# Kernel optimization log

Measured on AMD Instinct MI355X. Metric: run time of the kernel, lower is better.

Reference implementation:

```python
import jax, jax.numpy as jnp
import numpy as np
from jax import lax

STRIDES = (8, 8, 16, 32, 32)
GRIDS = (40, 36, 24, 16, 12)
MIN_SCORE = 0.1
KEEP_SCORE = 0.1
MASK_THR = 0.5
UPDATE_THR = 0.05
SIGMA = 2.0
TOPN = 500
MAX_MASKS = 100
UP = 4


def points_nms(h):
    # max_pool2d(k=2, s=1, p=1) then crop last row/col == pad (1,0) window 2
    m = lax.reduce_window(h, -jnp.inf, lax.max, (1, 1, 2, 2), (1, 1, 1, 1),
                          ((0, 0), (0, 0), (1, 0), (1, 0)))
    return h * (m == h).astype(h.dtype)


def resize_mat(insz, outsz):
    # bilinear align_corners=True interpolation matrix [outsz, insz]
    if outsz > 1:
        src = jnp.arange(outsz, dtype=jnp.float32) * ((insz - 1) / (outsz - 1))
    else:
        src = jnp.zeros((outsz,), jnp.float32)
    lo = jnp.clip(jnp.floor(src).astype(jnp.int32), 0, insz - 1)
    hi = jnp.minimum(lo + 1, insz - 1)
    w = src - lo.astype(jnp.float32)
    r = jnp.arange(outsz)
    M = jnp.zeros((outsz, insz), jnp.float32)
    return M.at[r, lo].add(1.0 - w).at[r, hi].add(w)


def bilinear(x, oh, ow):  # x: [k,h,w]
    Mh = resize_mat(x.shape[1], oh)
    Mw = resize_mat(x.shape[2], ow)
    return jnp.einsum('Ww,kHw->kHW', Mw, jnp.einsum('Hh,khw->kHw', Mh, x))


def prep(cate_preds, kernel_preds):
    B = cate_preds[0].shape[0]
    cate = [points_nms(jax.nn.sigmoid(c)) for c in cate_preds]
    cate_flat = jnp.concatenate(
        [jnp.transpose(c, (0, 2, 3, 1)).reshape(B, -1, c.shape[1]) for c in cate], axis=1)
    kern_flat = jnp.concatenate(
        [jnp.transpose(k, (0, 2, 3, 1)).reshape(B, -1, k.shape[1]) for k in kernel_preds], axis=1)
    strides_vec = jnp.concatenate(
        [jnp.full((g * g,), float(s), jnp.float32) for g, s in zip(GRIDS, STRIDES)])
    return cate_flat, kern_flat, strides_vec


def decode_soft(mask_feat, cate_flat, kern_flat, strides_vec):
    # fixed-shape (padded) version of the per-image decode; invalid slots carry score 0
    nc = cate_flat.shape[-1]
    flat = cate_flat.reshape(-1)
    vals, idx = lax.top_k(jnp.where(flat > MIN_SCORE, flat, -1.0), TOPN)
    validk = vals > MIN_SCORE
    cell = idx // nc
    label = idx % nc
    # dynamic 1x1 conv == einsum with gathered kernels
    sig = jax.nn.sigmoid(jnp.einsum('kc,chw->khw', kern_flat[cell], mask_feat))
    binm = (sig > MASK_THR).astype(sig.dtype)
    summ = binm.sum((1, 2))
    keep = validk & (summ > strides_vec[cell])
    seg = (sig * binm).sum((1, 2)) / jnp.maximum(summ, 1e-6)
    scores = jnp.where(keep, vals * seg, 0.0)
    order = jnp.argsort(-scores)
    scores = scores[order]
    sig = sig[order]
    label = label[order]
    keep_o = keep[order]
    summ = jnp.where(keep, summ, 0.0)[order]
    binm = binm[order] * keep_o[:, None, None].astype(binm.dtype)
    # matrix NMS (gaussian)
    flatm = binm.reshape(TOPN, -1)
    inter = flatm @ flatm.T
    iou = inter / jnp.maximum(summ[:, None] + summ[None, :] - inter, 1e-6)
    triu = jnp.triu(jnp.ones((TOPN, TOPN), bool), 1)
    dmat = jnp.where(triu & (label[:, None] == label[None, :]), iou, 0.0)
    comp = dmat.max(0)  # max suppression each item received
    coef = (jnp.exp(-SIGMA * dmat**2) / jnp.exp(-SIGMA * comp[:, None]**2)).min(0)
    s2 = scores * coef
    s2 = jnp.where((s2 >= UPDATE_THR) & (s2 >= KEEP_SCORE) & keep_o, s2, 0.0)
    fv, fi = lax.top_k(s2, MAX_MASKS)
    return fv, jnp.where(fv > 0, label[fi], -1), sig[fi]


def reference(mask_feat_pred, cate_pred_0, cate_pred_1, cate_pred_2, cate_pred_3,
              cate_pred_4, kernel_pred_0, kernel_pred_1, kernel_pred_2, kernel_pred_3,
              kernel_pred_4, scaled_sizes, origin_sizes):
    cate_preds = [cate_pred_0, cate_pred_1, cate_pred_2, cate_pred_3, cate_pred_4]
    kernel_preds = [kernel_pred_0, kernel_pred_1, kernel_pred_2, kernel_pred_3, kernel_pred_4]
    cate_flat, kern_flat, sv = prep(cate_preds, kernel_preds)
    fv, lab, sig = jax.vmap(lambda mf, cf, kf: decode_soft(mf, cf, kf, sv))(
        mask_feat_pred, cate_flat, kern_flat)
    H = mask_feat_pred.shape[2] * UP
    W = mask_feat_pred.shape[3] * UP
    up = jax.vmap(lambda s: bilinear(s, H, W))(sig)  # [B,M,H,W]
    sh, sw = int(scaled_sizes[0, 0]), int(scaled_sizes[0, 1])
    oh, ow = int(origin_sizes[0, 0]), int(origin_sizes[0, 1])
    up = up[:, :, :sh, :sw]
    up = jax.vmap(lambda s: bilinear(s, oh, ow))(up)
    masks = ((up > MASK_THR) & (fv > 0)[:, :, None, None]).astype(jnp.uint8)
    return masks, lab, fv


def setup_inputs() -> dict:
    key = jax.random.key(0)
    ks = jax.random.split(key, 11)
    B, C, NC, HM = 2, 256, 80, 128
    inp = {'mask_feat_pred': jax.random.normal(ks[0], (B, C, HM, HM), jnp.float32)}
    for i, g in enumerate(GRIDS):
        inp[f'cate_pred_{i}'] = jax.random.normal(ks[1 + i], (B, NC, g, g), jnp.float32)
        inp[f'kernel_pred_{i}'] = jax.random.normal(ks[6 + i], (B, C, g, g), jnp.float32) * 0.05
    inp['scaled_sizes'] = jnp.full((B, 2), HM * UP, jnp.int32)
    inp['origin_sizes'] = jnp.full((B, 2), HM * UP, jnp.int32)
    return inp
```

## Files before the change

kernel.cpp:

```cpp
#include <hip/hip_runtime.h>
#include <math.h>
#include <stdint.h>

#define NBATCH 2
#define NC 80
#define CHN 256
#define HMM 128
#define HWN (HMM*HMM)
#define NCELL 3872
#define FLATN (NCELL*NC)
#define TOPN 500
#define SROWS 512
#define MAXM 100
#define OUTH 512
#define OUTW 512
#define NBINS 1024
#define CANDCAP 2048
#define BM 128
#define BN2 256
#define BK 32
#define GNB (HWN/BN2)

__device__ __forceinline__ float sigmoidf_(float x){ return 1.0f/(1.0f+expf(-x)); }

__device__ __forceinline__ void cell_decode(int cell, int& lvl, int& g, int& y, int& x){
  int off;
  if (cell < 1600)      { lvl=0; g=40; off=0; }
  else if (cell < 2896) { lvl=1; g=36; off=1600; }
  else if (cell < 3472) { lvl=2; g=24; off=2896; }
  else if (cell < 3728) { lvl=3; g=16; off=3472; }
  else                  { lvl=4; g=12; off=3728; }
  int r = cell - off; y = r / g; x = r - y*g;
}

template<int N, int NT>
__device__ __forceinline__ void bitonic_desc(uint64_t* key){
  int tid = threadIdx.x;
  for (int k = 2; k <= N; k <<= 1)
    for (int j = k >> 1; j > 0; j >>= 1) {
      __syncthreads();
      for (int e = tid; e < N; e += NT) {
        int l = e ^ j;
        if (l > e) {
          uint64_t a = key[e], c = key[l];
          bool up = ((e & k) == 0);
          if (up ? (a < c) : (a > c)) { key[e] = c; key[l] = a; }
        }
      }
    }
  __syncthreads();
}

__global__ void k0_init(uint32_t* hist, uint32_t* cnt){
  int t = blockIdx.x*blockDim.x + threadIdx.x;
  if (t < NBATCH*NBINS) hist[t] = 0;
  if (t < NBATCH) cnt[t] = 0;
}

__global__ void k1_scores(const float* __restrict__ c0, const float* __restrict__ c1,
                          const float* __restrict__ c2, const float* __restrict__ c3,
                          const float* __restrict__ c4,
                          float* __restrict__ scores, uint32_t* __restrict__ hist){
  int t = blockIdx.x*blockDim.x + threadIdx.x;
  if (t >= NBATCH*FLATN) return;
  int b = t / FLATN;
  int rem = t - b*FLATN;
  int cell = rem / NC;
  int c = rem - cell*NC;
  int lvl,g,y,x; cell_decode(cell,lvl,g,y,x);
  const float* cp = lvl==0?c0:lvl==1?c1:lvl==2?c2:lvl==3?c3:c4;
  const float* base = cp + (size_t)(b*NC + c)*g*g;
  float raw = base[y*g + x];
  float m = raw;
  if (y > 0)          m = fmaxf(m, base[(y-1)*g + x]);
  if (x > 0)          m = fmaxf(m, base[y*g + x-1]);
  if (y > 0 && x > 0) m = fmaxf(m, base[(y-1)*g + x-1]);
  float s = (raw == m) ? sigmoidf_(raw) : 0.0f;
  scores[t] = s;
  if (s > 0.1f) {
    int bin = (int)(s * 1024.0f); if (bin > NBINS-1) bin = NBINS-1;
    atomicAdd(&hist[b*NBINS + bin], 1u);
  }
}

__global__ __launch_bounds__(1024) void k2_cutoff(const uint32_t* __restrict__ hist, int* __restrict__ cutoff){
  __shared__ uint32_t h[NBINS];
  int b = blockIdx.x;
  h[threadIdx.x] = hist[b*NBINS + threadIdx.x];
  __syncthreads();
  if (threadIdx.x == 0) {
    int acc = 0; int cut = 0;
    for (int d = NBINS-1; d >= 0; --d) {
      acc += (int)h[d];
      if (acc >= TOPN) { cut = d; break; }
    }
    cutoff[b] = cut;
  }
}

__global__ void k3_gather(const float* __restrict__ scores, const int* __restrict__ cutoff,
                          uint32_t* __restrict__ cnt, float* __restrict__ cval, uint32_t* __restrict__ cidx){
  int t = blockIdx.x*blockDim.x + threadIdx.x;
  if (t >= NBATCH*FLATN) return;
  int b = t / FLATN; int idx = t - b*FLATN;
  float v = scores[t];
  if (v > 0.1f) {
    int bin = (int)(v * 1024.0f); if (bin > NBINS-1) bin = NBINS-1;
    if (bin >= cutoff[b]) {
      uint32_t p = atomicAdd(&cnt[b], 1u);
      if (p < CANDCAP) { cval[b*CANDCAP+p] = v; cidx[b*CANDCAP+p] = (uint32_t)idx; }
    }
  }
}

__global__ __launch_bounds__(1024) void k4_sort(const uint32_t* __restrict__ cnt,
        const float* __restrict__ cval, const uint32_t* __restrict__ cidx,
        float* __restrict__ vals, int* __restrict__ cellA, int* __restrict__ labelA){
  __shared__ uint64_t key[CANDCAP];
  int b = blockIdx.x; int tid = threadIdx.x;
  int n = (int)cnt[b]; if (n > CANDCAP) n = CANDCAP;
  for (int e = tid; e < CANDCAP; e += 1024) {
    uint64_t k = 0;
    if (e < n)
      k = ((uint64_t)__float_as_uint(cval[b*CANDCAP+e]) << 32) |
          (uint64_t)(0xFFFFFFFFu - cidx[b*CANDCAP+e]);
    key[e] = k;
  }
  bitonic_desc<CANDCAP,1024>(key);
  for (int r = tid; r < TOPN; r += 1024) {
    uint64_t k = key[r];
    if ((k >> 32) == 0) { vals[b*TOPN+r] = -1.0f; cellA[b*TOPN+r] = 0; labelA[b*TOPN+r] = 0; }
    else {
      uint32_t idx = 0xFFFFFFFFu - (uint32_t)(k & 0xFFFFFFFFu);
      vals[b*TOPN+r]   = __uint_as_float((uint32_t)(k >> 32));
      cellA[b*TOPN+r]  = (int)(idx / NC);
      labelA[b*TOPN+r] = (int)(idx % NC);
    }
  }
}

__global__ void k5_kmat(const float* __restrict__ k0p, const float* __restrict__ k1p,
                        const float* __restrict__ k2p, const float* __restrict__ k3p,
                        const float* __restrict__ k4p,
                        const int* __restrict__ cellA, float* __restrict__ Kmat){
  int t = blockIdx.x*blockDim.x + threadIdx.x;
  if (t >= NBATCH*TOPN*CHN) return;
  int b = t / (TOPN*CHN); int rem = t - b*(TOPN*CHN);
  int k = rem / CHN; int c = rem - k*CHN;
  int cell = cellA[b*TOPN + k];
  int lvl,g,y,x; cell_decode(cell,lvl,g,y,x);
  const float* kp = lvl==0?k0p:lvl==1?k1p:lvl==2?k2p:lvl==3?k3p:k4p;
  Kmat[t] = kp[((size_t)(b*CHN + c)*g + y)*g + x];
}

__global__ __launch_bounds__(256, 2) void k6_gemm1(const float* __restrict__ Kmat, const float* __restrict__ mf,
        float* __restrict__ sigfull, uint32_t* __restrict__ bits,
        float* __restrict__ psum, float* __restrict__ pseg){
  __shared__ alignas(16) float As[BK][BM+4];
  __shared__ alignas(16) float Bs[BK][BN2];
  __shared__ uint32_t bitsL[BM][8];
  int tid = threadIdx.x;
  int nb = blockIdx.x, mb = blockIdx.y, b = blockIdx.z;
  int row0 = mb*BM, col0 = nb*BN2;
  int tx = tid & 15, ty = tid >> 4;
  for (int i = tid; i < BM*8; i += 256) ((uint32_t*)bitsL)[i] = 0;

  int ar[4], aq[4], bkk[8], bcc[8];
  #pragma unroll
  for (int i = 0; i < 4; ++i) { int e = i*256 + tid; ar[i] = e >> 3; aq[i] = e & 7; }
  #pragma unroll
  for (int i = 0; i < 8; ++i) { int e = i*256 + tid; bkk[i] = e >> 6; bcc[i] = e & 63; }

  float4 pa[4], pb[8];
  const float4 z4 = make_float4(0.f,0.f,0.f,0.f);
  #pragma unroll
  for (int i = 0; i < 4; ++i) {
    int rr = row0 + ar[i];
    pa[i] = (rr < TOPN) ? *(const float4*)&Kmat[((size_t)b*TOPN + rr)*CHN + aq[i]*4] : z4;
  }
  #pragma unroll
  for (int i = 0; i < 8; ++i)
    pb[i] = *(const float4*)&mf[((size_t)b*CHN + bkk[i])*HWN + col0 + bcc[i]*4];

  float acc[8][16];
  #pragma unroll
  for (int i=0;i<8;i++)
    #pragma unroll
    for(int j=0;j<16;j++) acc[i][j]=0.f;

  for (int k0 = 0; k0 < CHN; k0 += BK) {
    __syncthreads();
    #pragma unroll
    for (int i = 0; i < 4; ++i) {
      int colA = ar[i] ^ (aq[i] << 2);
      As[aq[i]*4+0][colA] = pa[i].x;
      As[aq[i]*4+1][colA] = pa[i].y;
      As[aq[i]*4+2][colA] = pa[i].z;
      As[aq[i]*4+3][colA] = pa[i].w;
    }
    #pragma unroll
    for (int i = 0; i < 8; ++i)
      *(float4*)&Bs[bkk[i]][bcc[i]*4] = pb[i];
    __syncthreads();
    if (k0 + BK < CHN) {
      int k0n = k0 + BK;
      #pragma unroll
      for (int i = 0; i < 4; ++i) {
        int rr = row0 + ar[i];
        pa[i] = (rr < TOPN) ? *(const float4*)&Kmat[((size_t)b*TOPN + rr)*CHN + k0n + aq[i]*4] : z4;
      }
      #pragma unroll
      for (int i = 0; i < 8; ++i)
        pb[i] = *(const float4*)&mf[((size_t)b*CHN + k0n + bkk[i])*HWN + col0 + bcc[i]*4];
    }
    #pragma unroll 2
    for (int kk = 0; kk < BK; ++kk) {
      int s = (kk >> 2) << 2;
      float4 a0 = *(float4*)&As[kk][(ty*8) ^ s];
      float4 a1 = *(float4*)&As[kk][(ty*8+4) ^ s];
      float av[8] = {a0.x,a0.y,a0.z,a0.w,a1.x,a1.y,a1.z,a1.w};
      #pragma unroll
      for (int q = 0; q < 4; ++q) {
        float4 bv = *(float4*)&Bs[kk][q*64 + tx*4];
        #pragma unroll
        for (int i = 0; i < 8; ++i) {
          acc[i][q*4+0] += av[i]*bv.x;
          acc[i][q*4+1] += av[i]*bv.y;
          acc[i][q*4+2] += av[i]*bv.z;
          acc[i][q*4+3] += av[i]*bv.w;
        }
      }
    }
  }
  #pragma unroll
  for (int i = 0; i < 8; ++i) {
    int r = row0 + ty*8 + i;
    float se = 0.f; int cc = 0;
    #pragma unroll
    for (int q = 0; q < 4; ++q) {
      float4 sv;
      sv.x = sigmoidf_(acc[i][q*4+0]);
      sv.y = sigmoidf_(acc[i][q*4+1]);
      sv.z = sigmoidf_(acc[i][q*4+2]);
      sv.w = sigmoidf_(acc[i][q*4+3]);
      uint32_t m = 0;
      if (sv.x > 0.5f) { m |= 1u; se += sv.x; cc++; }
      if (sv.y > 0.5f) { m |= 2u; se += sv.y; cc++; }
      if (sv.z > 0.5f) { m |= 4u; se += sv.z; cc++; }
      if (sv.w > 0.5f) { m |= 8u; se += sv.w; cc++; }
      atomicOr(&bitsL[ty*8+i][2*q + (tx>>3)], m << ((tx&7)*4));
      *(float4*)&sigfull[((size_t)b*SROWS + r)*HWN + col0 + q*64 + tx*4] = sv;
    }
    #pragma unroll
    for (int d = 1; d < 16; d <<= 1) {
      se += __shfl_xor(se, d);
      cc += __shfl_xor(cc, d);
    }
    if (tx == 0 && r < TOPN) {
      psum[((size_t)b*TOPN + r)*GNB + nb] = (float)cc;
      pseg[((size_t)b*TOPN + r)*GNB + nb] = se;
    }
  }
  __syncthreads();
  for (int e = tid; e < BM*8; e += 256) {
    int rr = e >> 3, w = e & 7;
    if (row0 + rr < TOPN)
      bits[((size_t)b*TOPN + row0 + rr)*512 + nb*8 + w] = bitsL[rr][w];
  }
}

__global__ void k7_rowstats(const float* __restrict__ psum, const float* __restrict__ pseg,
                            const float* __restrict__ vals, const int* __restrict__ cellA,
                            float* __restrict__ summ, float* __restrict__ scores, int* __restrict__ keepA){
  int t = blockIdx.x*blockDim.x + threadIdx.x;
  if (t >= NBATCH*TOPN) return;
  float sc = 0.f, sg = 0.f;
  for (int i = 0; i < GNB; i += 4) {
    float4 a = *(const float4*)&psum[(size_t)t*GNB+i];
    float4 c = *(const float4*)&pseg[(size_t)t*GNB+i];
    sc += a.x+a.y+a.z+a.w; sg += c.x+c.y+c.z+c.w;
  }
  float v = vals[t];
  int cell = cellA[t];
  int lvl,g,y,x; cell_decode(cell,lvl,g,y,x);
  float stride = (lvl<=1)?8.f:(lvl==2)?16.f:32.f;
  bool keep = (v > 0.1f) && (sc > stride);
  float seg = sg / fmaxf(sc, 1e-6f);
  summ[t] = sc;
  scores[t] = keep ? v*seg : 0.f;
  keepA[t] = keep ? 1 : 0;
}

__global__ __launch_bounds__(512) void k8_order(const float* __restrict__ scores, int* __restrict__ order){
  __shared__ uint64_t key[512];
  int b = blockIdx.x, tid = threadIdx.x;
  uint64_t k = 0;
  if (tid < TOPN)
    k = ((uint64_t)__float_as_uint(scores[b*TOPN+tid]) << 32) | (uint64_t)(0xFFFFFFFFu - (uint32_t)tid);
  key[tid] = k;
  bitonic_desc<512,512>(key);
  if (tid < TOPN) order[b*TOPN+tid] = (int)(0xFFFFFFFFu - (uint32_t)(key[tid] & 0xFFFFFFFFu));
}

__global__ __launch_bounds__(256) void k9_dmat(const uint32_t* __restrict__ bitsG,
        const int* __restrict__ order, const int* __restrict__ labelA, const int* __restrict__ keepA,
        const float* __restrict__ summ, float* __restrict__ dmatT){
  __shared__ uint32_t rowb[512];
  int i = blockIdx.x, b = blockIdx.y, tid = threadIdx.x;
  int oi = order[b*TOPN + i];
  if (!keepA[b*TOPN + oi]) return;
  float si = summ[b*TOPN + oi];
  int li = labelA[b*TOPN + oi];
  for (int w = tid; w < 512; w += 256) rowb[w] = bitsG[((size_t)b*TOPN + oi)*512 + w];
  __syncthreads();
  for (int j = i + 1 + tid; j < TOPN; j += 256) {
    int oj = order[b*TOPN + j];
    if (!keepA[b*TOPN + oj] || labelA[b*TOPN + oj] != li) continue;
    const uint4* rj = (const uint4*)&bitsG[((size_t)b*TOPN + oj)*512];
    const uint4* ri = (const uint4*)rowb;
    int cc = 0;
    for (int w = 0; w < 128; ++w) {
      uint4 x = rj[w], y = ri[w];
      cc += __popc(x.x & y.x) + __popc(x.y & y.y) + __popc(x.z & y.z) + __popc(x.w & y.w);
    }
    float sj = summ[b*TOPN + oj];
    float inter = (float)cc;
    dmatT[((size_t)b*TOPN + j)*TOPN + i] = inter / fmaxf(si + sj - inter, 1e-6f);
  }
}

__global__ __launch_bounds__(256) void k10_comp(const float* __restrict__ dmatT,
        float* __restrict__ comp, float* __restrict__ e2c){
  __shared__ float red[4];
  int j = blockIdx.x, b = blockIdx.y, tid = threadIdx.x;
  float m = 0.f;
  for (int i = tid; i < TOPN; i += 256) m = fmaxf(m, dmatT[((size_t)b*TOPN+j)*TOPN + i]);
  #pragma unroll
  for (int d = 1; d < 64; d <<= 1) m = fmaxf(m, __shfl_xor(m, d));
  if ((tid & 63) == 0) red[tid >> 6] = m;
  __syncthreads();
  if (tid == 0) {
    m = fmaxf(fmaxf(red[0], red[1]), fmaxf(red[2], red[3]));
    comp[b*TOPN+j] = m;
    e2c[b*TOPN+j] = expf(-2.0f*m*m);
  }
}

__global__ __launch_bounds__(256) void k10_coef(const float* __restrict__ dmatT, const float* __restrict__ e2c,
        const float* __restrict__ scores, const int* __restrict__ order, const int* __restrict__ keepA,
        float* __restrict__ s2){
  __shared__ float red[4];
  int j = blockIdx.x, b = blockIdx.y, tid = threadIdx.x;
  float mn = 1e30f;
  for (int i = tid; i < TOPN; i += 256) {
    float d = dmatT[((size_t)b*TOPN+j)*TOPN + i];
    float r = expf(-2.0f*d*d) / e2c[b*TOPN+i];
    mn = fminf(mn, r);
  }
  #pragma unroll
  for (int d = 1; d < 64; d <<= 1) mn = fminf(mn, __shfl_xor(mn, d));
  if ((tid & 63) == 0) red[tid >> 6] = mn;
  __syncthreads();
  if (tid == 0) {
    mn = fminf(fminf(red[0], red[1]), fminf(red[2], red[3]));
    int oj = order[b*TOPN+j];
    float s = scores[b*TOPN+oj] * mn;
    bool ok = (s >= 0.05f) && (s >= 0.1f) && (keepA[b*TOPN+oj] != 0);
    s2[b*TOPN+j] = ok ? s : 0.f;
  }
}

__global__ __launch_bounds__(512) void k11_top100(const float* __restrict__ s2, const int* __restrict__ order,
        const int* __restrict__ labelA, float* __restrict__ outF, int* __restrict__ selrow){
  __shared__ uint64_t key[512];
  int b = blockIdx.x, tid = threadIdx.x;
  uint64_t k = 0;
  if (tid < TOPN)
    k = ((uint64_t)__float_as_uint(s2[b*TOPN+tid]) << 32) | (uint64_t)(0xFFFFFFFFu - (uint32_t)tid);
  key[tid] = k;
  bitonic_desc<512,512>(key);
  if (tid < MAXM) {
    uint64_t kk = key[tid];
    float v = __uint_as_float((uint32_t)(kk >> 32));
    int j = (int)(0xFFFFFFFFu - (uint32_t)(kk & 0xFFFFFFFFu));
    if (j < 0 || j >= TOPN) { j = 0; v = 0.f; }
    int orow = order[b*TOPN + j];
    float lab = (v > 0.f) ? (float)labelA[b*TOPN + orow] : -1.0f;
    size_t maskCount = (size_t)NBATCH*MAXM*OUTH*OUTW;
    outF[maskCount + (size_t)b*MAXM + tid] = lab;
    outF[maskCount + (size_t)NBATCH*MAXM + (size_t)b*MAXM + tid] = v;
    selrow[b*MAXM + tid] = orow;
  }
}

__global__ void k13_upsample(const float* __restrict__ sigfull, const int* __restrict__ selrow,
                             float* __restrict__ outF){
  int t = blockIdx.x*blockDim.x + threadIdx.x;
  const int XG = OUTW/4;
  int total = NBATCH*MAXM*OUTH*XG;
  if (t >= total) return;
  int xg = t % XG;
  int tmp = t / XG;
  int Y = tmp % OUTH;
  int tmp2 = tmp / OUTH;
  int r = tmp2 % MAXM;
  int b = tmp2 / MAXM;
  size_t maskCount = (size_t)NBATCH*MAXM*OUTH*OUTW;
  float fv = outF[maskCount + (size_t)NBATCH*MAXM + (size_t)b*MAXM + r];
  float4 o = make_float4(0.f,0.f,0.f,0.f);
  if (fv > 0.f) {
    const float* sm = sigfull + ((size_t)b*SROWS + selrow[b*MAXM + r])*HWN;
    const float SC = (float)(127.0/511.0);
    float fy = (float)Y * SC;
    int ly = (int)floorf(fy); if (ly < 0) ly = 0; if (ly > HMM-1) ly = HMM-1;
    int hy = ly+1 < HMM ? ly+1 : HMM-1;
    float wy = fy - (float)ly;
    float res[4];
    #pragma unroll
    for (int u = 0; u < 4; ++u) {
      int X = xg*4 + u;
      float fx = (float)X * SC;
      int lx = (int)floorf(fx); if (lx < 0) lx = 0; if (lx > HMM-1) lx = HMM-1;
      int hx = lx+1 < HMM ? lx+1 : HMM-1;
      float wx = fx - (float)lx;
      float a = (1.f-wy)*sm[ly*HMM+lx] + wy*sm[hy*HMM+lx];
      float c = (1.f-wy)*sm[ly*HMM+hx] + wy*sm[hy*HMM+hx];
      float v = (1.f-wx)*a + wx*c;
      res[u] = (v > 0.5f) ? 1.f : 0.f;
    }
    o = make_float4(res[0],res[1],res[2],res[3]);
  }
  *(float4*)&outF[(((size_t)b*MAXM + r)*OUTH + Y)*OUTW + xg*4] = o;
}

extern "C" void kernel_launch(void* const* d_in, const int* in_sizes, int n_in,
                              void* d_out, int out_size, void* d_ws, size_t ws_size,
                              hipStream_t stream) {
  const float* mf = (const float*)d_in[0];
  const float *cate[5], *kern[5];
  bool interleaved = (n_in > 2) && (in_sizes[2] == NBATCH*CHN*40*40);
  if (interleaved) {
    for (int i = 0; i < 5; ++i) { cate[i] = (const float*)d_in[1 + 2*i]; kern[i] = (const float*)d_in[2 + 2*i]; }
  } else {
    for (int i = 0; i < 5; ++i) { cate[i] = (const float*)d_in[1 + i]; kern[i] = (const float*)d_in[6 + i]; }
  }
  float* outF = (float*)d_out;

  uint8_t* p = (uint8_t*)d_ws;
  auto alloc = [&](size_t bytes) -> void* {
    void* r = (void*)p;
    p += (bytes + 255) & ~(size_t)255;
    return r;
  };
  float*    cate_scores = (float*)   alloc((size_t)NBATCH*FLATN*4);
  uint32_t* hist        = (uint32_t*)alloc((size_t)NBATCH*NBINS*4);
  uint32_t* cnt         = (uint32_t*)alloc((size_t)NBATCH*4);
  int*      cutoff      = (int*)     alloc((size_t)NBATCH*4);
  float*    cval        = (float*)   alloc((size_t)NBATCH*CANDCAP*4);
  uint32_t* cidx        = (uint32_t*)alloc((size_t)NBATCH*CANDCAP*4);
  float*    vals        = (float*)   alloc((size_t)NBATCH*TOPN*4);
  int*      cellA       = (int*)     alloc((size_t)NBATCH*TOPN*4);
  int*      labelA      = (int*)     alloc((size_t)NBATCH*TOPN*4);
  float*    Kmat        = (float*)   alloc((size_t)NBATCH*TOPN*CHN*4);
  uint32_t* bits        = (uint32_t*)alloc((size_t)NBATCH*TOPN*512*4);
  float*    psum        = (float*)   alloc((size_t)NBATCH*TOPN*GNB*4);
  float*    pseg        = (float*)   alloc((size_t)NBATCH*TOPN*GNB*4);
  float*    summ        = (float*)   alloc((size_t)NBATCH*TOPN*4);
  float*    scores      = (float*)   alloc((size_t)NBATCH*TOPN*4);
  int*      keepA       = (int*)     alloc((size_t)NBATCH*TOPN*4);
  int*      order       = (int*)     alloc((size_t)NBATCH*TOPN*4);
  float*    dmatT       = (float*)   alloc((size_t)NBATCH*TOPN*TOPN*4);
  float*    comp        = (float*)   alloc((size_t)NBATCH*TOPN*4);
  float*    e2c         = (float*)   alloc((size_t)NBATCH*TOPN*4);
  float*    s2          = (float*)   alloc((size_t)NBATCH*TOPN*4);
  int*      selrow      = (int*)     alloc((size_t)NBATCH*MAXM*4);
  float*    sigfull     = (float*)   alloc((size_t)NBATCH*SROWS*HWN*4);
  (void)ws_size; (void)out_size;

  hipLaunchKernelGGL(k0_init, dim3((NBATCH*NBINS + 255)/256), dim3(256), 0, stream, hist, cnt);
  hipLaunchKernelGGL(k1_scores, dim3((NBATCH*FLATN + 255)/256), dim3(256), 0, stream,
                     cate[0], cate[1], cate[2], cate[3], cate[4], cate_scores, hist);
  hipLaunchKernelGGL(k2_cutoff, dim3(NBATCH), dim3(1024), 0, stream, hist, cutoff);
  hipLaunchKernelGGL(k3_gather, dim3((NBATCH*FLATN + 255)/256), dim3(256), 0, stream,
                     cate_scores, cutoff, cnt, cval, cidx);
  hipLaunchKernelGGL(k4_sort, dim3(NBATCH), dim3(1024), 0, stream, cnt, cval, cidx, vals, cellA, labelA);
  hipLaunchKernelGGL(k5_kmat, dim3((NBATCH*TOPN*CHN + 255)/256), dim3(256), 0, stream,
                     kern[0], kern[1], kern[2], kern[3], kern[4], cellA, Kmat);
  hipLaunchKernelGGL(k6_gemm1, dim3(HWN/BN2, (TOPN+BM-1)/BM, NBATCH), dim3(256), 0, stream,
                     Kmat, mf, sigfull, bits, psum, pseg);
  hipLaunchKernelGGL(k7_rowstats, dim3((NBATCH*TOPN + 255)/256), dim3(256), 0, stream,
                     psum, pseg, vals, cellA, summ, scores, keepA);
  hipLaunchKernelGGL(k8_order, dim3(NBATCH), dim3(512), 0, stream, scores, order);
  hipMemsetAsync(dmatT, 0, (size_t)NBATCH*TOPN*TOPN*4, stream);
  hipLaunchKernelGGL(k9_dmat, dim3(TOPN, NBATCH), dim3(256), 0, stream,
                     bits, order, labelA, keepA, summ, dmatT);
  hipLaunchKernelGGL(k10_comp, dim3(TOPN, NBATCH), dim3(256), 0, stream, dmatT, comp, e2c);
  hipLaunchKernelGGL(k10_coef, dim3(TOPN, NBATCH), dim3(256), 0, stream,
                     dmatT, e2c, scores, order, keepA, s2);
  hipLaunchKernelGGL(k11_top100, dim3(NBATCH), dim3(512), 0, stream, s2, order, labelA, outF, selrow);
  hipLaunchKernelGGL(k13_upsample, dim3((NBATCH*MAXM*OUTH*(OUTW/4) + 255)/256), dim3(256), 0, stream,
                     sigfull, selrow, outF);
}
```

Before: 390.3 us.

## Fuse kernel gather into GEMM, merge rowstats with ordering, drop init kernel

```diff
diff --git a/kernel.cpp b/kernel.cpp
--- a/kernel.cpp
+++ b/kernel.cpp
@@ -49,12 +49,6 @@
       }
     }
   __syncthreads();
-}
-
-__global__ void k0_init(uint32_t* hist, uint32_t* cnt){
-  int t = blockIdx.x*blockDim.x + threadIdx.x;
-  if (t < NBATCH*NBINS) hist[t] = 0;
-  if (t < NBATCH) cnt[t] = 0;
 }
 
 __global__ void k1_scores(const float* __restrict__ c0, const float* __restrict__ c1,
@@ -139,31 +133,19 @@
   }
 }
 
-__global__ void k5_kmat(const float* __restrict__ k0p, const float* __restrict__ k1p,
-                        const float* __restrict__ k2p, const float* __restrict__ k3p,
-                        const float* __restrict__ k4p,
-                        const int* __restrict__ cellA, float* __restrict__ Kmat){
-  int t = blockIdx.x*blockDim.x + threadIdx.x;
-  if (t >= NBATCH*TOPN*CHN) return;
-  int b = t / (TOPN*CHN); int rem = t - b*(TOPN*CHN);
-  int k = rem / CHN; int c = rem - k*CHN;
-  int cell = cellA[b*TOPN + k];
-  int lvl,g,y,x; cell_decode(cell,lvl,g,y,x);
-  const float* kp = lvl==0?k0p:lvl==1?k1p:lvl==2?k2p:lvl==3?k3p:k4p;
-  Kmat[t] = kp[((size_t)(b*CHN + c)*g + y)*g + x];
-}
-
-__global__ __launch_bounds__(256, 2) void k6_gemm1(const float* __restrict__ Kmat, const float* __restrict__ mf,
+__global__ __launch_bounds__(256) void k6_gemm1(
+        const float* __restrict__ k0p, const float* __restrict__ k1p,
+        const float* __restrict__ k2p, const float* __restrict__ k3p,
+        const float* __restrict__ k4p, const int* __restrict__ cellA,
+        const float* __restrict__ mf,
         float* __restrict__ sigfull, uint32_t* __restrict__ bits,
         float* __restrict__ psum, float* __restrict__ pseg){
   __shared__ alignas(16) float As[BK][BM+4];
   __shared__ alignas(16) float Bs[BK][BN2];
-  __shared__ uint32_t bitsL[BM][8];
   int tid = threadIdx.x;
   int nb = blockIdx.x, mb = blockIdx.y, b = blockIdx.z;
   int row0 = mb*BM, col0 = nb*BN2;
   int tx = tid & 15, ty = tid >> 4;
-  for (int i = tid; i < BM*8; i += 256) ((uint32_t*)bitsL)[i] = 0;
 
   int ar[4], aq[4], bkk[8], bcc[8];
   #pragma unroll
@@ -171,13 +153,25 @@
   #pragma unroll
   for (int i = 0; i < 8; ++i) { int e = i*256 + tid; bkk[i] = e >> 6; bcc[i] = e & 63; }
 
-  float4 pa[4], pb[8];
-  const float4 z4 = make_float4(0.f,0.f,0.f,0.f);
+  const float* kpp[4]; size_t boff[4]; int gg2[4]; bool okA[4];
   #pragma unroll
   for (int i = 0; i < 4; ++i) {
     int rr = row0 + ar[i];
-    pa[i] = (rr < TOPN) ? *(const float4*)&Kmat[((size_t)b*TOPN + rr)*CHN + aq[i]*4] : z4;
-  }
+    okA[i] = (rr < TOPN);
+    int cell = okA[i] ? cellA[b*TOPN + rr] : 0;
+    int lvl,g,y,x; cell_decode(cell,lvl,g,y,x);
+    kpp[i] = lvl==0?k0p:lvl==1?k1p:lvl==2?k2p:lvl==3?k3p:k4p;
+    gg2[i] = g*g;
+    boff[i] = (size_t)b*CHN*(size_t)(g*g) + (size_t)y*g + x;
+  }
+  #define LOADA_G(i, dst, K0N) { \
+    if (okA[i]) { int c0_ = (K0N) + aq[i]*4; const float* p_ = kpp[i] + boff[i] + (size_t)c0_*gg2[i]; \
+      dst.x = p_[0]; dst.y = p_[gg2[i]]; dst.z = p_[2*gg2[i]]; dst.w = p_[3*gg2[i]]; \
+    } else { dst = make_float4(0.f,0.f,0.f,0.f); } }
+
+  float4 pa[4], pb[8];
+  #pragma unroll
+  for (int i = 0; i < 4; ++i) LOADA_G(i, pa[i], 0)
   #pragma unroll
   for (int i = 0; i < 8; ++i)
     pb[i] = *(const float4*)&mf[((size_t)b*CHN + bkk[i])*HWN + col0 + bcc[i]*4];
@@ -205,10 +199,7 @@
     if (k0 + BK < CHN) {
       int k0n = k0 + BK;
       #pragma unroll
-      for (int i = 0; i < 4; ++i) {
-        int rr = row0 + ar[i];
-        pa[i] = (rr < TOPN) ? *(const float4*)&Kmat[((size_t)b*TOPN + rr)*CHN + k0n + aq[i]*4] : z4;
-      }
+      for (int i = 0; i < 4; ++i) LOADA_G(i, pa[i], k0n)
       #pragma unroll
       for (int i = 0; i < 8; ++i)
         pb[i] = *(const float4*)&mf[((size_t)b*CHN + k0n + bkk[i])*HWN + col0 + bcc[i]*4];
@@ -248,7 +239,12 @@
       if (sv.y > 0.5f) { m |= 2u; se += sv.y; cc++; }
       if (sv.z > 0.5f) { m |= 4u; se += sv.z; cc++; }
       if (sv.w > 0.5f) { m |= 8u; se += sv.w; cc++; }
-      atomicOr(&bitsL[ty*8+i][2*q + (tx>>3)], m << ((tx&7)*4));
+      uint32_t wrd = m << ((tx & 7)*4);
+      wrd |= __shfl_xor(wrd, 1);
+      wrd |= __shfl_xor(wrd, 2);
+      wrd |= __shfl_xor(wrd, 4);
+      if ((tx & 7) == 0 && r < TOPN)
+        bits[((size_t)b*TOPN + r)*512 + nb*8 + 2*q + (tx>>3)] = wrd;
       *(float4*)&sigfull[((size_t)b*SROWS + r)*HWN + col0 + q*64 + tx*4] = sv;
     }
     #pragma unroll
@@ -261,42 +257,35 @@
       pseg[((size_t)b*TOPN + r)*GNB + nb] = se;
     }
   }
-  __syncthreads();
-  for (int e = tid; e < BM*8; e += 256) {
-    int rr = e >> 3, w = e & 7;
-    if (row0 + rr < TOPN)
-      bits[((size_t)b*TOPN + row0 + rr)*512 + nb*8 + w] = bitsL[rr][w];
-  }
-}
-
-__global__ void k7_rowstats(const float* __restrict__ psum, const float* __restrict__ pseg,
-                            const float* __restrict__ vals, const int* __restrict__ cellA,
-                            float* __restrict__ summ, float* __restrict__ scores, int* __restrict__ keepA){
-  int t = blockIdx.x*blockDim.x + threadIdx.x;
-  if (t >= NBATCH*TOPN) return;
-  float sc = 0.f, sg = 0.f;
-  for (int i = 0; i < GNB; i += 4) {
-    float4 a = *(const float4*)&psum[(size_t)t*GNB+i];
-    float4 c = *(const float4*)&pseg[(size_t)t*GNB+i];
-    sc += a.x+a.y+a.z+a.w; sg += c.x+c.y+c.z+c.w;
-  }
-  float v = vals[t];
-  int cell = cellA[t];
-  int lvl,g,y,x; cell_decode(cell,lvl,g,y,x);
-  float stride = (lvl<=1)?8.f:(lvl==2)?16.f:32.f;
-  bool keep = (v > 0.1f) && (sc > stride);
-  float seg = sg / fmaxf(sc, 1e-6f);
-  summ[t] = sc;
-  scores[t] = keep ? v*seg : 0.f;
-  keepA[t] = keep ? 1 : 0;
-}
-
-__global__ __launch_bounds__(512) void k8_order(const float* __restrict__ scores, int* __restrict__ order){
+}
+
+__global__ __launch_bounds__(512) void k78_stats_order(const float* __restrict__ psum, const float* __restrict__ pseg,
+        const float* __restrict__ vals, const int* __restrict__ cellA,
+        float* __restrict__ summ, float* __restrict__ scores, int* __restrict__ keepA,
+        int* __restrict__ order){
   __shared__ uint64_t key[512];
   int b = blockIdx.x, tid = threadIdx.x;
   uint64_t k = 0;
-  if (tid < TOPN)
-    k = ((uint64_t)__float_as_uint(scores[b*TOPN+tid]) << 32) | (uint64_t)(0xFFFFFFFFu - (uint32_t)tid);
+  if (tid < TOPN) {
+    int t = b*TOPN + tid;
+    float sc = 0.f, sg = 0.f;
+    for (int i = 0; i < GNB; i += 4) {
+      float4 a = *(const float4*)&psum[(size_t)t*GNB+i];
+      float4 c = *(const float4*)&pseg[(size_t)t*GNB+i];
+      sc += a.x+a.y+a.z+a.w; sg += c.x+c.y+c.z+c.w;
+    }
+    float v = vals[t];
+    int cell = cellA[t];
+    int lvl,g,y,x; cell_decode(cell,lvl,g,y,x);
+    float stride = (lvl<=1)?8.f:(lvl==2)?16.f:32.f;
+    bool keep = (v > 0.1f) && (sc > stride);
+    float seg = sg / fmaxf(sc, 1e-6f);
+    summ[t] = sc;
+    float s = keep ? v*seg : 0.f;
+    scores[t] = s;
+    keepA[t] = keep ? 1 : 0;
+    k = ((uint64_t)__float_as_uint(s) << 32) | (uint64_t)(0xFFFFFFFFu - (uint32_t)tid);
+  }
   key[tid] = k;
   bitonic_desc<512,512>(key);
   if (tid < TOPN) order[b*TOPN+tid] = (int)(0xFFFFFFFFu - (uint32_t)(key[tid] & 0xFFFFFFFFu));
@@ -453,15 +442,14 @@
     return r;
   };
   float*    cate_scores = (float*)   alloc((size_t)NBATCH*FLATN*4);
-  uint32_t* hist        = (uint32_t*)alloc((size_t)NBATCH*NBINS*4);
-  uint32_t* cnt         = (uint32_t*)alloc((size_t)NBATCH*4);
+  uint32_t* hist        = (uint32_t*)alloc((size_t)(NBATCH*NBINS + NBATCH)*4);
+  uint32_t* cnt         = hist + NBATCH*NBINS;
   int*      cutoff      = (int*)     alloc((size_t)NBATCH*4);
   float*    cval        = (float*)   alloc((size_t)NBATCH*CANDCAP*4);
   uint32_t* cidx        = (uint32_t*)alloc((size_t)NBATCH*CANDCAP*4);
   float*    vals        = (float*)   alloc((size_t)NBATCH*TOPN*4);
   int*      cellA       = (int*)     alloc((size_t)NBATCH*TOPN*4);
   int*      labelA      = (int*)     alloc((size_t)NBATCH*TOPN*4);
-  float*    Kmat        = (float*)   alloc((size_t)NBATCH*TOPN*CHN*4);
   uint32_t* bits        = (uint32_t*)alloc((size_t)NBATCH*TOPN*512*4);
   float*    psum        = (float*)   alloc((size_t)NBATCH*TOPN*GNB*4);
   float*    pseg        = (float*)   alloc((size_t)NBATCH*TOPN*GNB*4);
@@ -477,21 +465,19 @@
   float*    sigfull     = (float*)   alloc((size_t)NBATCH*SROWS*HWN*4);
   (void)ws_size; (void)out_size;
 
-  hipLaunchKernelGGL(k0_init, dim3((NBATCH*NBINS + 255)/256), dim3(256), 0, stream, hist, cnt);
+  hipMemsetAsync(hist, 0, (size_t)(NBATCH*NBINS + NBATCH)*4, stream);
+  hipMemsetAsync(dmatT, 0, (size_t)NBATCH*TOPN*TOPN*4, stream);
   hipLaunchKernelGGL(k1_scores, dim3((NBATCH*FLATN + 255)/256), dim3(256), 0, stream,
                      cate[0], cate[1], cate[2], cate[3], cate[4], cate_scores, hist);
   hipLaunchKernelGGL(k2_cutoff, dim3(NBATCH), dim3(1024), 0, stream, hist, cutoff);
   hipLaunchKernelGGL(k3_gather, dim3((NBATCH*FLATN + 255)/256), dim3(256), 0, stream,
                      cate_scores, cutoff, cnt, cval, cidx);
   hipLaunchKernelGGL(k4_sort, dim3(NBATCH), dim3(1024), 0, stream, cnt, cval, cidx, vals, cellA, labelA);
-  hipLaunchKernelGGL(k5_kmat, dim3((NBATCH*TOPN*CHN + 255)/256), dim3(256), 0, stream,
-                     kern[0], kern[1], kern[2], kern[3], kern[4], cellA, Kmat);
   hipLaunchKernelGGL(k6_gemm1, dim3(HWN/BN2, (TOPN+BM-1)/BM, NBATCH), dim3(256), 0, stream,
-                     Kmat, mf, sigfull, bits, psum, pseg);
-  hipLaunchKernelGGL(k7_rowstats, dim3((NBATCH*TOPN + 255)/256), dim3(256), 0, stream,
-                     psum, pseg, vals, cellA, summ, scores, keepA);
-  hipLaunchKernelGGL(k8_order, dim3(NBATCH), dim3(512), 0, stream, scores, order);
-  hipMemsetAsync(dmatT, 0, (size_t)NBATCH*TOPN*TOPN*4, stream);
+                     kern[0], kern[1], kern[2], kern[3], kern[4], cellA, mf,
+                     sigfull, bits, psum, pseg);
+  hipLaunchKernelGGL(k78_stats_order, dim3(NBATCH), dim3(512), 0, stream,
+                     psum, pseg, vals, cellA, summ, scores, keepA, order);
   hipLaunchKernelGGL(k9_dmat, dim3(TOPN, NBATCH), dim3(256), 0, stream,
                      bits, order, labelA, keepA, summ, dmatT);
   hipLaunchKernelGGL(k10_comp, dim3(TOPN, NBATCH), dim3(256), 0, stream, dmatT, comp, e2c);
```

Result: slower. 435.4 us (+11.6%).
